# Kernel optimization log

Measured on AMD Instinct MI355X. Metric: run time of the kernel, lower is better.

## Reference

```python
import jax, jax.numpy as jnp
import numpy as np

IOU_THRESHOLD = 0.5
OBJ_WEIGHT = 0.5


def setup_inputs() -> dict:
    key = jax.random.key(0)
    k0, k1, k2, k3, k4 = jax.random.split(key, 5)
    b, t, a = 64, 60, 3
    det0 = jax.random.normal(k0, (b, a, 160, 160, 5), jnp.float32)
    det1 = jax.random.normal(k1, (b, a, 80, 80, 5), jnp.float32)
    det2 = jax.random.normal(k2, (b, a, 40, 40, 5), jnp.float32)
    # scaled anchors in grid-cell units, (s=3 scales, a=3 anchors, wh)
    anchors = jax.random.uniform(k3, (3, a, 2), jnp.float32, 1.0, 10.0)
    # normalized target boxes (x, y, w, h) in [0, 1)
    targets = jax.random.uniform(k4, (b, t, 4), jnp.float32)
    return {"det0": det0, "det1": det1, "det2": det2, "anchors": anchors, "targets": targets}


def _calc_overlap(anchors, zt):
    # anchors: (s, a, 2); zt: (b, t, s, 4) -> iou-like overlap (b, t, s, a)
    s, a = anchors.shape[:2]
    b, t = zt.shape[:2]
    anc = anchors.reshape(1, 1, s, a, 2)
    tg = zt.reshape(b, t, s, 1, 4)
    lb = jnp.maximum(-anc / 2, tg[..., 0:2] - tg[..., 2:4] / 2)
    ub = jnp.minimum(anc / 2, tg[..., 0:2] + tg[..., 2:4] / 2)
    m = jnp.prod((lb < ub).astype(anc.dtype), axis=4)
    inter = jnp.prod(ub - lb, axis=4) * m
    anc_area = jnp.prod(anc, axis=4)                       # (1,1,s,a)
    tgt_area = (tg[..., 2] - tg[..., 0]) * (tg[..., 3] - tg[..., 1])  # (b,t,s,1), faithful to source
    return inter / (anc_area + tgt_area - inter)


def _suppress(overlap, thr):
    # faithful to the sequential in-place edits in suppress_anchors
    b, t, s, a = overlap.shape
    ov = overlap.reshape(b * t, s * a)
    mx = jnp.max(ov, axis=1, keepdims=True)
    ov = jnp.where(ov == mx, 1.0, ov)
    ov = jnp.where(ov < thr, 0.0, ov)
    ov = jnp.where((ov != 0.0) & (ov != 1.0), -1.0, ov)
    return ov.reshape(b, t, s, a)


def _object_loss(det0, det1, det2, anchors, targets):
    preds = [det0, det1, det2]
    b, t = targets.shape[:2]
    s, a = anchors.shape[:2]
    shapes = np.array([(p.shape[2], p.shape[3]) for p in preds])  # (s, 2) static (h, w)
    shapes_f = jnp.asarray(shapes, dtype=targets.dtype)

    mask_flat = jnp.all(targets[..., 0:4] != -1, axis=2).reshape(-1)  # (b*t,)

    # target cells: (cy, cx) = floor((ty, tx) * (h, w)) per scale -> (b, t, s, 2)
    yx = jnp.stack([targets[..., 1], targets[..., 0]], axis=-1)  # (b, t, 2)
    cells = (yx[:, :, None, :] * shapes_f[None, None, :, :]).astype(jnp.int32)

    # zeroed targets: scale by (w, h, w, h), center offsets in [-0.5, 0.5)
    whwh = shapes_f[:, jnp.array([1, 0, 1, 0])]  # (s, 4)
    zt = targets[..., 0:4][:, :, None, :] * whwh[None, None, :, :]  # (b, t, s, 4)
    xy = zt[..., 0:2] - (jnp.floor(zt[..., 0:2]) + 0.5)
    zt = jnp.concatenate([xy, zt[..., 2:4]], axis=-1)

    gt_values = _suppress(_calc_overlap(anchors, zt), IOU_THRESHOLD)  # (b, t, s, a)

    bidx = jnp.repeat(jnp.arange(b, dtype=jnp.int32), t)  # (b*t,)
    aidx = jnp.arange(a, dtype=jnp.int32)[None, :]        # (1, a)

    gt_flat = []
    for si, p in enumerate(preds):
        h, w = int(shapes[si, 0]), int(shapes[si, 1])
        cy = cells[:, :, si, 0].reshape(-1)
        cx = cells[:, :, si, 1].reshape(-1)
        cy = jnp.where(mask_flat, cy, h)  # invalid targets -> out of range -> dropped
        vals = gt_values[:, :, si, :].reshape(-1, a)  # (b*t, a)
        gt = jnp.zeros((b, a, h, w), dtype=targets.dtype)
        gt = gt.at[bidx[:, None], aidx, cy[:, None], cx[:, None]].set(vals, mode='drop')
        gt_flat.append(gt.reshape(-1))

    ground_truth = jnp.concatenate(gt_flat, axis=0)
    logits = jnp.concatenate([p[..., 4].reshape(-1) for p in preds], axis=0)

    # BCEWithLogitsLoss with pos_weight pw: (1-y)*x + (1 + (pw-1)*y) * softplus(-x), mean
    y = ground_truth
    x = logits
    loss = jnp.mean((1.0 - y) * x + (1.0 + (OBJ_WEIGHT - 1.0) * y) * jax.nn.softplus(-x))
    return loss


def reference(det0, det1, det2, anchors, targets):
    return _object_loss(det0, det1, det2, anchors, targets)
```

## Files before the change

### kernel.cpp

```cpp
#include <hip/hip_runtime.h>
#include <math.h>

#define B 64
#define T 60
#define NA 3
#define NS 3
#define BT (B*T)
#define NB_SCAN 2048
#define NB_CORR ((BT + 255) / 256)
#define NB_ALL (NB_SCAN + NB_CORR)
#define NTHREADS (NB_SCAN * 256)
#define N_TOTAL 6451200.0f

#define G4_0 6144000
#define G4_1 1536000
#define G4_2 384000

__device__ __forceinline__ float softplus_f(float x) {
    float e = __expf(-fabsf(x));
    return fmaxf(x, 0.0f) + __logf(1.0f + e);
}

__device__ __forceinline__ float pick(float4 f, int ph) {
    return (ph == 1) ? f.x : (ph == 2) ? f.y : (ph == 3) ? f.z : f.w;
}

__device__ __forceinline__ float block_reduce_sum(float v) {
    for (int o = 32; o > 0; o >>= 1) v += __shfl_down(v, o, 64);
    __shared__ float s[4];
    int lane = threadIdx.x & 63;
    int w = threadIdx.x >> 6;
    if (lane == 0) s[w] = v;
    __syncthreads();
    if (threadIdx.x == 0) {
        float t = 0.0f;
        #pragma unroll
        for (int i = 0; i < 4; ++i) t += s[i];
        return t;
    }
    return 0.0f;
}

__device__ __forceinline__ float scan_tensor(const float4* __restrict__ p,
                                             int n4, int tid) {
    float acc = 0.0f;
    int i = tid;
    int phase = tid % 5;
    while (i + 3 * NTHREADS < n4) {
        float4 f0 = p[i];
        float4 f1 = p[i + NTHREADS];
        float4 f2 = p[i + 2 * NTHREADS];
        float4 f3 = p[i + 3 * NTHREADS];
        int p0 = phase;
        int p1 = p0 + 3; if (p1 >= 5) p1 -= 5;
        int p2 = p1 + 3; if (p2 >= 5) p2 -= 5;
        int p3 = p2 + 3; if (p3 >= 5) p3 -= 5;
        if (p0) acc += softplus_f(pick(f0, p0));
        if (p1) acc += softplus_f(pick(f1, p1));
        if (p2) acc += softplus_f(pick(f2, p2));
        if (p3) acc += softplus_f(pick(f3, p3));
        phase = p3 + 3; if (phase >= 5) phase -= 5;
        i += 4 * NTHREADS;
    }
    for (; i < n4; i += NTHREADS) {
        float4 f = p[i];
        if (phase) acc += softplus_f(pick(f, phase));
        phase += 3; if (phase >= 5) phase -= 5;
    }
    return acc;
}

__global__ void __launch_bounds__(256, 8) fused_main_kernel(
    const float* __restrict__ d0, const float* __restrict__ d1,
    const float* __restrict__ d2, const float* __restrict__ anchors,
    const float* __restrict__ targets, float* __restrict__ partials) {
    float acc = 0.0f;

    if (blockIdx.x < NB_SCAN) {
        int tid = blockIdx.x * 256 + threadIdx.x;
        acc = scan_tensor((const float4*)d0, G4_0, tid)
            + scan_tensor((const float4*)d1, G4_1, tid)
            + scan_tensor((const float4*)d2, G4_2, tid);
    } else {
        int tid = (blockIdx.x - NB_SCAN) * 256 + threadIdx.x;
        if (tid < BT) {
            int bi = tid / T;
            const float* tg = targets + tid * 4;
            float tx = tg[0], ty = tg[1], tw = tg[2], th = tg[3];
            bool mask = (tx != -1.0f) && (ty != -1.0f) &&
                        (tw != -1.0f) && (th != -1.0f);
            const int dims[NS] = {160, 80, 40};
            const float* dets[NS] = {d0, d1, d2};

            float ov[NS][NA];
            float mx = -INFINITY;
            #pragma unroll
            for (int si = 0; si < NS; ++si) {
                float D = (float)dims[si];
                float ztx = tx * D, zty = ty * D, ztw = tw * D, zth = th * D;
                float fx = ztx - (floorf(ztx) + 0.5f);
                float fy = zty - (floorf(zty) + 0.5f);
                float tarea = (ztw - fx) * (zth - fy);
                #pragma unroll
                for (int ai = 0; ai < NA; ++ai) {
                    float a0 = anchors[(si * NA + ai) * 2 + 0];
                    float a1 = anchors[(si * NA + ai) * 2 + 1];
                    float lb0 = fmaxf(-0.5f * a0, fx - 0.5f * ztw);
                    float ub0 = fminf( 0.5f * a0, fx + 0.5f * ztw);
                    float lb1 = fmaxf(-0.5f * a1, fy - 0.5f * zth);
                    float ub1 = fminf( 0.5f * a1, fy + 0.5f * zth);
                    float m = ((lb0 < ub0) && (lb1 < ub1)) ? 1.0f : 0.0f;
                    float inter = (ub0 - lb0) * (ub1 - lb1) * m;
                    float v = inter / (a0 * a1 + tarea - inter);
                    ov[si][ai] = v;
                    mx = fmaxf(mx, v);
                }
            }
            if (mask) {
                #pragma unroll
                for (int si = 0; si < NS; ++si) {
                    int D = dims[si];
                    int cy = (int)(ty * (float)D);
                    int cx = (int)(tx * (float)D);
                    if (cy >= 0 && cy < D && cx >= 0 && cx < D) {
                        #pragma unroll
                        for (int ai = 0; ai < NA; ++ai) {
                            float v = ov[si][ai];
                            float y = (v == mx) ? 1.0f
                                    : ((v < 0.5f) ? 0.0f : -1.0f);
                            if (y != 0.0f) {
                                long idx = ((((long)bi * NA + ai) * D + cy) * D + cx) * 5 + 4;
                                float x = dets[si][idx];
                                acc += -y * x - 0.5f * y * softplus_f(-x);
                            }
                        }
                    }
                }
            }
        }
    }

    float bs = block_reduce_sum(acc);
    if (threadIdx.x == 0) partials[blockIdx.x] = bs;
}

__global__ void __launch_bounds__(256) final_kernel(
    const float* __restrict__ wsf, float* __restrict__ out) {
    float acc = 0.0f;
    for (int i = threadIdx.x; i < NB_ALL; i += blockDim.x)
        acc += wsf[i];
    float bs = block_reduce_sum(acc);
    if (threadIdx.x == 0) out[0] = bs / N_TOTAL;
}

extern "C" void kernel_launch(void* const* d_in, const int* in_sizes, int n_in,
                              void* d_out, int out_size, void* d_ws, size_t ws_size,
                              hipStream_t stream) {
    const float* det0    = (const float*)d_in[0];
    const float* det1    = (const float*)d_in[1];
    const float* det2    = (const float*)d_in[2];
    const float* anchors = (const float*)d_in[3];
    const float* targets = (const float*)d_in[4];
    float* out = (float*)d_out;
    float* wsf = (float*)d_ws;

    fused_main_kernel<<<NB_ALL, 256, 0, stream>>>(det0, det1, det2,
                                                  anchors, targets, wsf);
    final_kernel<<<1, 256, 0, stream>>>(wsf, out);
}
```

Before: 30.62 us.

## Flatten scan across all tensors and fold final reduction into last block

The three per-tensor strided scans become one flat index space over all three detection tensors. Each thread issues fixed groups of five float4 loads, which keeps the phase pattern constant per thread and removes the loop-carried phase updates. The separate final reduction kernel is replaced by an atomic ticket, so the last block to finish sums the partials, at the cost of a memset before the launch. The per-element branch that picks the source tensor adds some address arithmetic.

```diff
diff --git a/kernel.cpp b/kernel.cpp
--- a/kernel.cpp
+++ b/kernel.cpp
@@ -9,12 +9,15 @@
 #define NB_SCAN 2048
 #define NB_CORR ((BT + 255) / 256)
 #define NB_ALL (NB_SCAN + NB_CORR)
-#define NTHREADS (NB_SCAN * 256)
+#define NT 524288
 #define N_TOTAL 6451200.0f
 
 #define G4_0 6144000
 #define G4_1 1536000
 #define G4_2 384000
+#define FLAT4 (G4_0 + G4_1 + G4_2)
+#define K_FULL 15
+#define REM_START (K_FULL * NT)
 
 __device__ __forceinline__ float softplus_f(float x) {
     float e = __expf(-fabsf(x));
@@ -23,6 +26,15 @@
 
 __device__ __forceinline__ float pick(float4 f, int ph) {
     return (ph == 1) ? f.x : (ph == 2) ? f.y : (ph == 3) ? f.z : f.w;
+}
+
+__device__ __forceinline__ float4 load_flat(const float4* __restrict__ d0,
+                                            const float4* __restrict__ d1,
+                                            const float4* __restrict__ d2,
+                                            int idx) {
+    if (idx < G4_0) return d0[idx];
+    if (idx < G4_0 + G4_1) return d1[idx - G4_0];
+    return d2[idx - (G4_0 + G4_1)];
 }
 
 __device__ __forceinline__ float block_reduce_sum(float v) {
@@ -41,46 +53,41 @@
     return 0.0f;
 }
 
-__device__ __forceinline__ float scan_tensor(const float4* __restrict__ p,
-                                             int n4, int tid) {
+__global__ void __launch_bounds__(256, 8) fused_main_kernel(
+    const float* __restrict__ d0f, const float* __restrict__ d1f,
+    const float* __restrict__ d2f, const float* __restrict__ anchors,
+    const float* __restrict__ targets, float* __restrict__ partials,
+    unsigned* __restrict__ ticket, float* __restrict__ out) {
+    const float4* d0 = (const float4*)d0f;
+    const float4* d1 = (const float4*)d1f;
+    const float4* d2 = (const float4*)d2f;
     float acc = 0.0f;
-    int i = tid;
-    int phase = tid % 5;
-    while (i + 3 * NTHREADS < n4) {
-        float4 f0 = p[i];
-        float4 f1 = p[i + NTHREADS];
-        float4 f2 = p[i + 2 * NTHREADS];
-        float4 f3 = p[i + 3 * NTHREADS];
-        int p0 = phase;
+
+    if (blockIdx.x < NB_SCAN) {
+        int g0 = blockIdx.x * 256 + threadIdx.x;
+        int p0 = g0 % 5;
         int p1 = p0 + 3; if (p1 >= 5) p1 -= 5;
         int p2 = p1 + 3; if (p2 >= 5) p2 -= 5;
         int p3 = p2 + 3; if (p3 >= 5) p3 -= 5;
-        if (p0) acc += softplus_f(pick(f0, p0));
-        if (p1) acc += softplus_f(pick(f1, p1));
-        if (p2) acc += softplus_f(pick(f2, p2));
-        if (p3) acc += softplus_f(pick(f3, p3));
-        phase = p3 + 3; if (phase >= 5) phase -= 5;
-        i += 4 * NTHREADS;
-    }
-    for (; i < n4; i += NTHREADS) {
-        float4 f = p[i];
-        if (phase) acc += softplus_f(pick(f, phase));
-        phase += 3; if (phase >= 5) phase -= 5;
-    }
-    return acc;
-}
-
-__global__ void __launch_bounds__(256, 8) fused_main_kernel(
-    const float* __restrict__ d0, const float* __restrict__ d1,
-    const float* __restrict__ d2, const float* __restrict__ anchors,
-    const float* __restrict__ targets, float* __restrict__ partials) {
-    float acc = 0.0f;
-
-    if (blockIdx.x < NB_SCAN) {
-        int tid = blockIdx.x * 256 + threadIdx.x;
-        acc = scan_tensor((const float4*)d0, G4_0, tid)
-            + scan_tensor((const float4*)d1, G4_1, tid)
-            + scan_tensor((const float4*)d2, G4_2, tid);
+        int p4 = p3 + 3; if (p4 >= 5) p4 -= 5;
+        #pragma unroll
+        for (int grp = 0; grp < 3; ++grp) {
+            int base = g0 + grp * 5 * NT;
+            float4 f0 = load_flat(d0, d1, d2, base);
+            float4 f1 = load_flat(d0, d1, d2, base + NT);
+            float4 f2 = load_flat(d0, d1, d2, base + 2 * NT);
+            float4 f3 = load_flat(d0, d1, d2, base + 3 * NT);
+            float4 f4 = load_flat(d0, d1, d2, base + 4 * NT);
+            if (p0) acc += softplus_f(pick(f0, p0));
+            if (p1) acc += softplus_f(pick(f1, p1));
+            if (p2) acc += softplus_f(pick(f2, p2));
+            if (p3) acc += softplus_f(pick(f3, p3));
+            if (p4) acc += softplus_f(pick(f4, p4));
+        }
+        if (g0 < FLAT4 - REM_START) {
+            float4 f = load_flat(d0, d1, d2, g0 + REM_START);
+            if (p0) acc += softplus_f(pick(f, p0));
+        }
     } else {
         int tid = (blockIdx.x - NB_SCAN) * 256 + threadIdx.x;
         if (tid < BT) {
@@ -90,7 +97,7 @@
             bool mask = (tx != -1.0f) && (ty != -1.0f) &&
                         (tw != -1.0f) && (th != -1.0f);
             const int dims[NS] = {160, 80, 40};
-            const float* dets[NS] = {d0, d1, d2};
+            const float* dets[NS] = {d0f, d1f, d2f};
 
             float ov[NS][NA];
             float mx = -INFINITY;
@@ -141,16 +148,23 @@
     }
 
     float bs = block_reduce_sum(acc);
-    if (threadIdx.x == 0) partials[blockIdx.x] = bs;
-}
 
-__global__ void __launch_bounds__(256) final_kernel(
-    const float* __restrict__ wsf, float* __restrict__ out) {
-    float acc = 0.0f;
-    for (int i = threadIdx.x; i < NB_ALL; i += blockDim.x)
-        acc += wsf[i];
-    float bs = block_reduce_sum(acc);
-    if (threadIdx.x == 0) out[0] = bs / N_TOTAL;
+    __shared__ bool is_last;
+    if (threadIdx.x == 0) {
+        partials[blockIdx.x] = bs;
+        __threadfence();
+        unsigned t = atomicAdd(ticket, 1u);
+        is_last = (t == NB_ALL - 1);
+    }
+    __syncthreads();
+    if (is_last) {
+        __threadfence();
+        float a2 = 0.0f;
+        for (int i = threadIdx.x; i < NB_ALL; i += 256)
+            a2 += ((volatile float*)partials)[i];
+        float tot = block_reduce_sum(a2);
+        if (threadIdx.x == 0) out[0] = tot / N_TOTAL;
+    }
 }
 
 extern "C" void kernel_launch(void* const* d_in, const int* in_sizes, int n_in,
@@ -163,8 +177,10 @@
     const float* targets = (const float*)d_in[4];
     float* out = (float*)d_out;
     float* wsf = (float*)d_ws;
+    unsigned* ticket = (unsigned*)(wsf + NB_ALL);
 
+    hipMemsetAsync(ticket, 0, sizeof(unsigned), stream);
     fused_main_kernel<<<NB_ALL, 256, 0, stream>>>(det0, det1, det2,
-                                                  anchors, targets, wsf);
-    final_kernel<<<1, 256, 0, stream>>>(wsf, out);
+                                                  anchors, targets,
+                                                  wsf, ticket, out);
 }
```

Measured after the change: 93.32 us. +204.8%, slower.

## Partition scan blocks per tensor with fixed fifteen-load stride pattern

Applied to the files above, without the earlier changes.

Splits the streaming softplus scan across dedicated block pools sized for each detection tensor (1600/400/100 blocks) instead of every thread striding over all three tensors. Strides are chosen as multiples of 5 so each thread's float4 phase within the 5-float record stays constant. Each thread then does exactly 15 loads with no loop bounds checks, and threads whose phase is 0 skip all loads. This removes per-iteration phase arithmetic and tail loops, but it idles one fifth of the threads and still reads only one useful float per float4, so the kernel remains bandwidth bound.

```diff
diff --git a/kernel.cpp b/kernel.cpp
--- a/kernel.cpp
+++ b/kernel.cpp
@@ -6,15 +6,17 @@
 #define NA 3
 #define NS 3
 #define BT (B*T)
-#define NB_SCAN 2048
+
+#define NB0 1600
+#define NB1 400
+#define NB2 100
+#define NB_SCAN (NB0 + NB1 + NB2)
 #define NB_CORR ((BT + 255) / 256)
 #define NB_ALL (NB_SCAN + NB_CORR)
-#define NTHREADS (NB_SCAN * 256)
+#define POOL0 (NB0 * 256)
+#define POOL1 (NB1 * 256)
+#define POOL2 (NB2 * 256)
 #define N_TOTAL 6451200.0f
-
-#define G4_0 6144000
-#define G4_1 1536000
-#define G4_2 384000
 
 __device__ __forceinline__ float softplus_f(float x) {
     float e = __expf(-fabsf(x));
@@ -41,46 +43,44 @@
     return 0.0f;
 }
 
-__device__ __forceinline__ float scan_tensor(const float4* __restrict__ p,
-                                             int n4, int tid) {
+__device__ __forceinline__ float scan15(const float4* __restrict__ p,
+                                        int g0, int stride) {
     float acc = 0.0f;
-    int i = tid;
-    int phase = tid % 5;
-    while (i + 3 * NTHREADS < n4) {
-        float4 f0 = p[i];
-        float4 f1 = p[i + NTHREADS];
-        float4 f2 = p[i + 2 * NTHREADS];
-        float4 f3 = p[i + 3 * NTHREADS];
-        int p0 = phase;
-        int p1 = p0 + 3; if (p1 >= 5) p1 -= 5;
-        int p2 = p1 + 3; if (p2 >= 5) p2 -= 5;
-        int p3 = p2 + 3; if (p3 >= 5) p3 -= 5;
-        if (p0) acc += softplus_f(pick(f0, p0));
-        if (p1) acc += softplus_f(pick(f1, p1));
-        if (p2) acc += softplus_f(pick(f2, p2));
-        if (p3) acc += softplus_f(pick(f3, p3));
-        phase = p3 + 3; if (phase >= 5) phase -= 5;
-        i += 4 * NTHREADS;
-    }
-    for (; i < n4; i += NTHREADS) {
-        float4 f = p[i];
-        if (phase) acc += softplus_f(pick(f, phase));
-        phase += 3; if (phase >= 5) phase -= 5;
+    int phase = g0 % 5;
+    if (phase) {
+        #pragma unroll
+        for (int grp = 0; grp < 3; ++grp) {
+            int base = g0 + (5 * grp) * stride;
+            float4 f0 = p[base];
+            float4 f1 = p[base + stride];
+            float4 f2 = p[base + 2 * stride];
+            float4 f3 = p[base + 3 * stride];
+            float4 f4 = p[base + 4 * stride];
+            acc += softplus_f(pick(f0, phase));
+            acc += softplus_f(pick(f1, phase));
+            acc += softplus_f(pick(f2, phase));
+            acc += softplus_f(pick(f3, phase));
+            acc += softplus_f(pick(f4, phase));
+        }
     }
     return acc;
 }
 
 __global__ void __launch_bounds__(256, 8) fused_main_kernel(
-    const float* __restrict__ d0, const float* __restrict__ d1,
-    const float* __restrict__ d2, const float* __restrict__ anchors,
+    const float* __restrict__ d0f, const float* __restrict__ d1f,
+    const float* __restrict__ d2f, const float* __restrict__ anchors,
     const float* __restrict__ targets, float* __restrict__ partials) {
     float acc = 0.0f;
 
-    if (blockIdx.x < NB_SCAN) {
-        int tid = blockIdx.x * 256 + threadIdx.x;
-        acc = scan_tensor((const float4*)d0, G4_0, tid)
-            + scan_tensor((const float4*)d1, G4_1, tid)
-            + scan_tensor((const float4*)d2, G4_2, tid);
+    if (blockIdx.x < NB0) {
+        int g0 = blockIdx.x * 256 + threadIdx.x;
+        acc = scan15((const float4*)d0f, g0, POOL0);
+    } else if (blockIdx.x < NB0 + NB1) {
+        int g0 = (blockIdx.x - NB0) * 256 + threadIdx.x;
+        acc = scan15((const float4*)d1f, g0, POOL1);
+    } else if (blockIdx.x < NB_SCAN) {
+        int g0 = (blockIdx.x - NB0 - NB1) * 256 + threadIdx.x;
+        acc = scan15((const float4*)d2f, g0, POOL2);
     } else {
         int tid = (blockIdx.x - NB_SCAN) * 256 + threadIdx.x;
         if (tid < BT) {
@@ -90,7 +90,7 @@
             bool mask = (tx != -1.0f) && (ty != -1.0f) &&
                         (tw != -1.0f) && (th != -1.0f);
             const int dims[NS] = {160, 80, 40};
-            const float* dets[NS] = {d0, d1, d2};
+            const float* dets[NS] = {d0f, d1f, d2f};
 
             float ov[NS][NA];
             float mx = -INFINITY;
```

Result: no change. 30.85 us (+0.7%).
